# Optimization experiments

Measured on AMD Instinct MI355X. Metric: run time of the kernel, lower is better.

The kernel has to match this reference:

```python
import jax, jax.numpy as jnp
import numpy as np
import math

B, NV, L = 64, 21, 2048
PATCH, STRIDE = 16, 8
PNUM = (L - PATCH) // STRIDE + 1  # 255 patches
D, H, NDIM = 128, 256, 2
PRED = 96
EPS = 1e-5
SCALE = 1.0 / math.sqrt(NDIM)  # MultiHeadEMA scale = sqrt(1/ndim)
# patch gather indices: [PNUM, PATCH]
PIDX = np.arange(PNUM)[:, None] * STRIDE + np.arange(PATCH)[None, :]


def setup_inputs() -> dict:
    key = jax.random.key(0)
    ks = jax.random.split(key, 24)
    nrm = lambda k, shape, std: std * jax.random.normal(k, shape, jnp.float32)
    inp = {}
    inp['x'] = jax.random.normal(ks[0], (B, NV, L), jnp.float32)
    # LEMencoder feature_projection: LEMblock(PATCH -> H -> D)
    inp['fp_w1'] = nrm(ks[1], (PATCH, H), 0.1)
    inp['fp_b1'] = jnp.zeros((H,), jnp.float32)
    inp['fp_w2'] = nrm(ks[2], (H, D), 0.1)
    inp['fp_b2'] = jnp.zeros((D,), jnp.float32)
    inp['fp_wr'] = nrm(ks[3], (PATCH, D), 0.1)
    inp['fp_br'] = jnp.zeros((D,), jnp.float32)
    inp['fp_g'] = jnp.ones((D,), jnp.float32)
    inp['fp_be'] = jnp.zeros((D,), jnp.float32)
    # 2 stacked encoder LEMblocks (D -> D -> D), leading layer axis
    inp['enc_w1'] = nrm(ks[4], (2, D, D), 0.05)
    inp['enc_b1'] = jnp.zeros((2, D), jnp.float32)
    inp['enc_w2'] = nrm(ks[5], (2, D, D), 0.05)
    inp['enc_b2'] = jnp.zeros((2, D), jnp.float32)
    inp['enc_wr'] = nrm(ks[6], (2, D, D), 0.05)
    inp['enc_br'] = jnp.zeros((2, D), jnp.float32)
    inp['enc_g'] = jnp.ones((2, D), jnp.float32)
    inp['enc_be'] = jnp.zeros((2, D), jnp.float32)
    # MultiHeadEMA params (unidirectional: kernel_dim == D)
    inp['ema_delta'] = nrm(ks[7], (D, NDIM, 1), 0.2)
    inp['ema_alpha'] = nrm(ks[8], (D, NDIM, 1), 0.2)
    val = jnp.array([1.0, -1.0], jnp.float32).reshape(1, NDIM, 1)  # +1/-1 alternating init
    inp['ema_beta'] = nrm(ks[9], (D, NDIM, 1), 0.02) + val
    inp['ema_gamma'] = nrm(ks[10], (D, NDIM), 1.0)
    inp['ema_omega'] = nrm(ks[11], (D,), 1.0)
    # Flatten_Head (shared): Linear(D*PNUM -> PRED)
    inp['head_w'] = nrm(ks[12], (D * PNUM, PRED), 0.02)
    inp['head_b'] = jnp.zeros((PRED,), jnp.float32)
    return inp


def _lemblock(x, w1, b1, w2, b2, wr, br, g, be):
    h = jax.nn.relu(x @ w1 + b1) @ w2 + b2
    y = h + (x @ wr + br)
    mu = jnp.mean(y, axis=-1, keepdims=True)
    var = jnp.mean(jnp.square(y - mu), axis=-1, keepdims=True)
    return g * (y - mu) * jax.lax.rsqrt(var + EPS) + be


def reference(x, fp_w1, fp_b1, fp_w2, fp_b2, fp_wr, fp_br, fp_g, fp_be,
              enc_w1, enc_b1, enc_w2, enc_b2, enc_wr, enc_br, enc_g, enc_be,
              ema_delta, ema_alpha, ema_beta, ema_gamma, ema_omega,
              head_w, head_b):
    # patching: [B, NV, L] -> [B*NV, PNUM, PATCH]
    z = x[:, :, PIDX].reshape(B * NV, PNUM, PATCH)
    # LEMencoder
    z = _lemblock(z, fp_w1, fp_b1, fp_w2, fp_b2, fp_wr, fp_br, fp_g, fp_be)
    for i in range(enc_w1.shape[0]):
        z = _lemblock(z, enc_w1[i], enc_b1[i], enc_w2[i], enc_b2[i],
                      enc_wr[i], enc_br[i], enc_g[i], enc_be[i])
    # MultiHeadEMA over patch (time) axis; input [Time=PNUM, Batch=B*NV, Channel=D]
    t = jnp.transpose(z, (1, 0, 2))
    residual = t * ema_omega
    xc = jnp.transpose(t, (1, 2, 0))  # [BN, D, PNUM]
    p = jax.nn.sigmoid(ema_delta)           # [D, N, 1]
    q = 1.0 - p * jax.nn.sigmoid(ema_alpha)  # [D, N, 1]
    vander = jnp.arange(PNUM, dtype=jnp.float32)[None, None, :] * jnp.log(q)  # [D, N, PNUM]
    kern = p * ema_beta * jnp.exp(vander)
    k = jnp.einsum('dnl,dn->dl', kern, ema_gamma * SCALE)  # [D, PNUM]
    n2 = 2 * PNUM
    out = jnp.fft.irfft(jnp.fft.rfft(xc, n=n2) * jnp.fft.rfft(k, n=n2), n=n2)[..., :PNUM]
    out = jax.nn.silu(jnp.transpose(out, (2, 0, 1)) + residual)  # [PNUM, BN, D]
    # Flatten_Head (shared): [B, NV, D, PNUM] -> flatten(-2) -> linear
    u = jnp.transpose(out, (1, 2, 0)).reshape(B, NV, D * PNUM)
    return u @ head_w + head_b  # [B, NV, PRED]
```

## Files before the change

### kernel.cpp

```cpp
#include <hip/hip_runtime.h>

typedef unsigned short u16;
typedef short bf8v __attribute__((ext_vector_type(8)));
typedef float f4v __attribute__((ext_vector_type(4)));
typedef float f16v __attribute__((ext_vector_type(16)));

#define DEV static __device__ __forceinline__

constexpr int BB   = 64;
constexpr int NV   = 21;
constexpr int BN   = BB * NV;
constexpr int PNUM = 255;
constexpr int D    = 128;
constexpr int PRED = 96;
constexpr int ROWS = BN * PNUM;
constexpr int KH   = D * PNUM;
constexpr int CH   = 30;
constexpr int KPC  = KH / CH;
constexpr int HITER = KPC / 32;
constexpr float EMA_SCALE = 0.70710678118654752440f;

DEV float bf2f(u16 h) { return __uint_as_float(((unsigned)h) << 16); }
DEV u16 f2bf(float f) {
  unsigned u = __float_as_uint(f);
  return (u16)((u + 0x7fffu + ((u >> 16) & 1u)) >> 16);
}
DEV unsigned pkbf2(float a, float b) {
  unsigned ua = __float_as_uint(a) + 0x8000u;
  unsigned ub = __float_as_uint(b) + 0x8000u;
  return __builtin_amdgcn_perm(ub, ua, 0x07060302u);
}
DEV bf8v mk4(unsigned a, unsigned b, unsigned c, unsigned d) {
  int4 t = {(int)a, (int)b, (int)c, (int)d};
  bf8v r;
  __builtin_memcpy(&r, &t, 16);
  return r;
}
DEV bf8v ld8(const u16* p) {
  bf8v r;
  __builtin_memcpy(&r, p, 16);
  return r;
}
DEV f4v mfma16(bf8v a, bf8v b, f4v c) {
  return __builtin_amdgcn_mfma_f32_16x16x32_bf16(a, b, c, 0, 0, 0);
}
DEV f16v mfma32(bf8v a, bf8v b, f16v c) {
  return __builtin_amdgcn_mfma_f32_32x32x16_bf16(a, b, c, 0, 0, 0);
}
DEV f16v zero16() {
  f16v r;
#pragma unroll
  for (int i = 0; i < 16; i++) r[i] = 0.f;
  return r;
}

#define FRG(pk, ks)                                                            \
  mk4(pk[(ks) >> 1][2 * ((ks) & 1)][0], pk[(ks) >> 1][2 * ((ks) & 1)][1],      \
      pk[(ks) >> 1][2 * ((ks) & 1) + 1][0], pk[(ks) >> 1][2 * ((ks) & 1) + 1][1])

__global__ void swz_all(
    const float* __restrict__ fw1, const float* __restrict__ fw2,
    const float* __restrict__ fwr, const float* __restrict__ ew1,
    const float* __restrict__ ew2, const float* __restrict__ ewr,
    const float* __restrict__ hw, u16* __restrict__ wb, u16* __restrict__ wsh) {
  int b = blockIdx.x;
  if (b >= 560) {
    int i = (b - 560) * 256 + threadIdx.x;
    if (i >= KH * PRED) return;
    int kp = i / PRED, n = i - kp * PRED;
    int l = kp >> 7, d = kp & 127;
    wsh[((size_t)(kp >> 3) * PRED + n) * 8 + (kp & 7)] =
        f2bf(hw[(size_t)(d * PNUM + l) * PRED + n]);
    return;
  }
  const float* src; u16* dst; int K, N, Kp;
  if (b < 32)       { src = fw1; dst = wb;          K = 16;  N = 256; Kp = 32; }
  else if (b < 160) { b -= 32;  src = fw2; dst = wb + 8192;  K = 256; N = 128; Kp = 256; }
  else if (b < 176) { b -= 160; src = fwr; dst = wb + 40960; K = 16;  N = 128; Kp = 32; }
  else {
    int e = (b - 176) >> 6; b = (b - 176) & 63;
    int l = e / 3, w = e - 3 * l;
    const float* basep = (w == 0) ? ew1 : (w == 1) ? ew2 : ewr;
    src = basep + (size_t)l * 16384;
    dst = wb + 45056 + e * 16384;
    K = 128; N = 128; Kp = 128;
  }
  int i = b * 256 + threadIdx.x;
  if (i >= Kp * N) return;
  int k = i / N, n = i - k * N;
  int np = (n & ~12) | ((n & 4) << 1) | ((n & 8) >> 1);
  u16 v = (k < K) ? f2bf(src[(size_t)k * N + np]) : (u16)0;
  dst[((size_t)(k >> 3) * N + n) * 8 + (k & 7)] = v;
}

__global__ __launch_bounds__(128, 2) void k_lem(
    const float* __restrict__ x,
    const u16* __restrict__ ws1, const float* __restrict__ b1,
    const u16* __restrict__ ws2, const u16* __restrict__ wsr,
    const float* __restrict__ b2, const float* __restrict__ br,
    const float* __restrict__ g, const float* __restrict__ be,
    const u16* __restrict__ wse, const float* __restrict__ eb1,
    const float* __restrict__ eb2, const float* __restrict__ ebr,
    const float* __restrict__ eg, const float* __restrict__ ebe,
    u16* __restrict__ zout) {
  __shared__ __align__(16) u16 zst[64 * 132];
  const int t = threadIdx.x;
  const int lane = t & 63, w = t >> 6;
  const int hh = lane >> 5, r5 = lane & 31;
  const int tile = blockIdx.x;
  const int row = tile * 64 + w * 32 + r5;

  bf8v azv;
  {
    unsigned R = (unsigned)row;
    unsigned bn = R / 255u;
    unsigned p = R - bn * 255u;
    const float* px = x + (size_t)bn * 2048u + p * 8u + hh * 8;
    float4 v0 = *(const float4*)px;
    float4 v1 = *(const float4*)(px + 4);
    azv = mk4(pkbf2(v0.x, v0.y), pkbf2(v0.z, v0.w),
              pkbf2(v1.x, v1.y), pkbf2(v1.z, v1.w));
  }

  unsigned hpk[8][4][2];
  unsigned zpk[4][4][2];

#pragma unroll
  for (int half = 0; half < 2; half++) {
    f16v a[4];
#pragma unroll
    for (int gg = 0; gg < 4; gg++) {
      bf8v wf = ld8(ws1 + ((size_t)(hh * 256 + (half * 4 + gg) * 32 + r5)) * 8);
      a[gg] = mfma32(wf, azv, zero16());
    }
#pragma unroll
    for (int gg = 0; gg < 4; gg++)
#pragma unroll
      for (int wq = 0; wq < 4; wq++) {
        int c0 = (half * 4 + gg) * 32 + ((wq >> 1) << 4) + ((wq & 1) << 2) + (hh << 3);
        float4 bv = *(const float4*)(b1 + c0);
        float v0 = fmaxf(a[gg][wq * 4 + 0] + bv.x, 0.f);
        float v1 = fmaxf(a[gg][wq * 4 + 1] + bv.y, 0.f);
        float v2 = fmaxf(a[gg][wq * 4 + 2] + bv.z, 0.f);
        float v3 = fmaxf(a[gg][wq * 4 + 3] + bv.w, 0.f);
        hpk[half * 4 + gg][wq][0] = pkbf2(v0, v1);
        hpk[half * 4 + gg][wq][1] = pkbf2(v2, v3);
      }
  }

  f16v acc[4];
  {
    {
      bf8v wr4[4];
#pragma unroll
      for (int gg = 0; gg < 4; gg++)
        wr4[gg] = ld8(wsr + ((size_t)(hh * 128 + gg * 32 + r5)) * 8);
#pragma unroll
      for (int gg = 0; gg < 4; gg++) acc[gg] = mfma32(wr4[gg], azv, zero16());
    }
    bf8v wq[2][4];
#pragma unroll
    for (int gg = 0; gg < 4; gg++)
      wq[0][gg] = ld8(ws2 + ((size_t)(hh * 128 + gg * 32 + r5)) * 8);
#pragma unroll
    for (int u = 0; u < 16; u++) {
      int cur = u & 1;
      if (u + 1 < 16) {
#pragma unroll
        for (int gg = 0; gg < 4; gg++)
          wq[cur ^ 1][gg] =
              ld8(ws2 + ((size_t)((2 * (u + 1) + hh) * 128 + gg * 32 + r5)) * 8);
      }
      bf8v bfr = FRG(hpk, u);
#pragma unroll
      for (int gg = 0; gg < 4; gg++) acc[gg] = mfma32(wq[cur][gg], bfr, acc[gg]);
    }
    float s = 0.f, s2 = 0.f;
#pragma unroll
    for (int gg = 0; gg < 4; gg++)
#pragma unroll
      for (int wq4 = 0; wq4 < 4; wq4++) {
        int c0 = gg * 32 + ((wq4 >> 1) << 4) + ((wq4 & 1) << 2) + (hh << 3);
        float4 bv2 = *(const float4*)(b2 + c0);
        float4 bvr = *(const float4*)(br + c0);
        acc[gg][wq4 * 4 + 0] += bv2.x + bvr.x;
        acc[gg][wq4 * 4 + 1] += bv2.y + bvr.y;
        acc[gg][wq4 * 4 + 2] += bv2.z + bvr.z;
        acc[gg][wq4 * 4 + 3] += bv2.w + bvr.w;
#pragma unroll
        for (int sidx = 0; sidx < 4; sidx++) {
          float v = acc[gg][wq4 * 4 + sidx];
          s += v; s2 += v * v;
        }
      }
    s += __shfl_xor(s, 32, 64); s2 += __shfl_xor(s2, 32, 64);
    float mean = s * (1.f / 128.f);
    float rstd = rsqrtf(s2 * (1.f / 128.f) - mean * mean + 1e-5f);
#pragma unroll
    for (int gg = 0; gg < 4; gg++)
#pragma unroll
      for (int wq4 = 0; wq4 < 4; wq4++) {
        int c0 = gg * 32 + ((wq4 >> 1) << 4) + ((wq4 & 1) << 2) + (hh << 3);
        float4 gv = *(const float4*)(g + c0);
        float4 bv = *(const float4*)(be + c0);
        float v0 = (acc[gg][wq4 * 4 + 0] - mean) * rstd * gv.x + bv.x;
        float v1 = (acc[gg][wq4 * 4 + 1] - mean) * rstd * gv.y + bv.y;
        float v2 = (acc[gg][wq4 * 4 + 2] - mean) * rstd * gv.z + bv.z;
        float v3 = (acc[gg][wq4 * 4 + 3] - mean) * rstd * gv.w + bv.w;
        zpk[gg][wq4][0] = pkbf2(v0, v1);
        zpk[gg][wq4][1] = pkbf2(v2, v3);
      }
  }

#pragma unroll 1
  for (int L = 0; L < 2; L++) {
    const u16* w1p = wse + (size_t)(L * 3 + 0) * 16384;
    const u16* w2p = wse + (size_t)(L * 3 + 1) * 16384;
    const u16* wrp = wse + (size_t)(L * 3 + 2) * 16384;
    unsigned hp2[4][4][2];
    {
      f16v a2[4];
#pragma unroll
      for (int gg = 0; gg < 4; gg++) a2[gg] = zero16();
      bf8v wq[2][4];
#pragma unroll
      for (int gg = 0; gg < 4; gg++)
        wq[0][gg] = ld8(w1p + ((size_t)(hh * 128 + gg * 32 + r5)) * 8);
#pragma unroll
      for (int u = 0; u < 8; u++) {
        int cur = u & 1;
        if (u + 1 < 8) {
#pragma unroll
          for (int gg = 0; gg < 4; gg++)
            wq[cur ^ 1][gg] =
                ld8(w1p + ((size_t)((2 * (u + 1) + hh) * 128 + gg * 32 + r5)) * 8);
        }
        bf8v bfr = FRG(zpk, u);
#pragma unroll
        for (int gg = 0; gg < 4; gg++) a2[gg] = mfma32(wq[cur][gg], bfr, a2[gg]);
      }
#pragma unroll
      for (int gg = 0; gg < 4; gg++)
#pragma unroll
        for (int wq4 = 0; wq4 < 4; wq4++) {
          int c0 = gg * 32 + ((wq4 >> 1) << 4) + ((wq4 & 1) << 2) + (hh << 3);
          float4 bv = *(const float4*)(eb1 + L * 128 + c0);
          float v0 = fmaxf(a2[gg][wq4 * 4 + 0] + bv.x, 0.f);
          float v1 = fmaxf(a2[gg][wq4 * 4 + 1] + bv.y, 0.f);
          float v2 = fmaxf(a2[gg][wq4 * 4 + 2] + bv.z, 0.f);
          float v3 = fmaxf(a2[gg][wq4 * 4 + 3] + bv.w, 0.f);
          hp2[gg][wq4][0] = pkbf2(v0, v1);
          hp2[gg][wq4][1] = pkbf2(v2, v3);
        }
    }
#pragma unroll
    for (int gg = 0; gg < 4; gg++) acc[gg] = zero16();
    {
      bf8v wq[2][4];
#pragma unroll
      for (int gg = 0; gg < 4; gg++)
        wq[0][gg] = ld8(w2p + ((size_t)(hh * 128 + gg * 32 + r5)) * 8);
#pragma unroll
      for (int u = 0; u < 8; u++) {
        int cur = u & 1;
        if (u + 1 < 8) {
#pragma unroll
          for (int gg = 0; gg < 4; gg++)
            wq[cur ^ 1][gg] =
                ld8(w2p + ((size_t)((2 * (u + 1) + hh) * 128 + gg * 32 + r5)) * 8);
        }
        bf8v bfr = FRG(hp2, u);
#pragma unroll
        for (int gg = 0; gg < 4; gg++) acc[gg] = mfma32(wq[cur][gg], bfr, acc[gg]);
      }
    }
    {
      bf8v wq[2][4];
#pragma unroll
      for (int gg = 0; gg < 4; gg++)
        wq[0][gg] = ld8(wrp + ((size_t)(hh * 128 + gg * 32 + r5)) * 8);
#pragma unroll
      for (int u = 0; u < 8; u++) {
        int cur = u & 1;
        if (u + 1 < 8) {
#pragma unroll
          for (int gg = 0; gg < 4; gg++)
            wq[cur ^ 1][gg] =
                ld8(wrp + ((size_t)((2 * (u + 1) + hh) * 128 + gg * 32 + r5)) * 8);
        }
        bf8v bfr = FRG(zpk, u);
#pragma unroll
        for (int gg = 0; gg < 4; gg++) acc[gg] = mfma32(wq[cur][gg], bfr, acc[gg]);
      }
    }
    float s = 0.f, s2 = 0.f;
#pragma unroll
    for (int gg = 0; gg < 4; gg++)
#pragma unroll
      for (int wq4 = 0; wq4 < 4; wq4++) {
        int c0 = gg * 32 + ((wq4 >> 1) << 4) + ((wq4 & 1) << 2) + (hh << 3);
        float4 bv2 = *(const float4*)(eb2 + L * 128 + c0);
        float4 bvr = *(const float4*)(ebr + L * 128 + c0);
        acc[gg][wq4 * 4 + 0] += bv2.x + bvr.x;
        acc[gg][wq4 * 4 + 1] += bv2.y + bvr.y;
        acc[gg][wq4 * 4 + 2] += bv2.z + bvr.z;
        acc[gg][wq4 * 4 + 3] += bv2.w + bvr.w;
#pragma unroll
        for (int sidx = 0; sidx < 4; sidx++) {
          float v = acc[gg][wq4 * 4 + sidx];
          s += v; s2 += v * v;
        }
      }
    s += __shfl_xor(s, 32, 64); s2 += __shfl_xor(s2, 32, 64);
    float mean = s * (1.f / 128.f);
    float rstd = rsqrtf(s2 * (1.f / 128.f) - mean * mean + 1e-5f);
#pragma unroll
    for (int gg = 0; gg < 4; gg++)
#pragma unroll
      for (int wq4 = 0; wq4 < 4; wq4++) {
        int c0 = gg * 32 + ((wq4 >> 1) << 4) + ((wq4 & 1) << 2) + (hh << 3);
        float4 gv = *(const float4*)(eg + L * 128 + c0);
        float4 bv = *(const float4*)(ebe + L * 128 + c0);
        float v0 = (acc[gg][wq4 * 4 + 0] - mean) * rstd * gv.x + bv.x;
        float v1 = (acc[gg][wq4 * 4 + 1] - mean) * rstd * gv.y + bv.y;
        float v2 = (acc[gg][wq4 * 4 + 2] - mean) * rstd * gv.z + bv.z;
        float v3 = (acc[gg][wq4 * 4 + 3] - mean) * rstd * gv.w + bv.w;
        unsigned plo = pkbf2(v0, v1), phi = pkbf2(v2, v3);
        if (L == 0) {
          zpk[gg][wq4][0] = plo;
          zpk[gg][wq4][1] = phi;
        } else {
          uint2 pv = {plo, phi};
          *(uint2*)(zst + (w * 32 + r5) * 132 + c0) = pv;
        }
      }
  }

#pragma unroll
  for (int it = 0; it < 8; it++) {
    int lu = it * 64 + lane;
    int rr = lu >> 4, seg = lu & 15;
    int orow = w * 32 + rr;
    *(uint4*)(zout + ((size_t)tile * 64 + orow) * 128 + seg * 8) =
        *(const uint4*)(zst + orow * 132 + seg * 8);
  }
}

__global__ __launch_bounds__(128) void k_ema(
    u16* __restrict__ z,
    const float* __restrict__ pdel, const float* __restrict__ palp,
    const float* __restrict__ pbet, const float* __restrict__ pgam,
    const float* __restrict__ pome) {
  __shared__ __align__(16) u16 zc[64 * 128];
  const int t = threadIdx.x;
  const int bn = blockIdx.x;
  float p0 = 1.f / (1.f + __expf(-pdel[t * 2 + 0]));
  float p1 = 1.f / (1.f + __expf(-pdel[t * 2 + 1]));
  float q0 = 1.f - p0 / (1.f + __expf(-palp[t * 2 + 0]));
  float q1 = 1.f - p1 / (1.f + __expf(-palp[t * 2 + 1]));
  float w0 = p0 * pbet[t * 2 + 0] * pgam[t * 2 + 0] * EMA_SCALE;
  float w1 = p1 * pbet[t * 2 + 1] * pgam[t * 2 + 1] * EMA_SCALE;
  float om = pome[t];
  float s0 = 0.f, s1 = 0.f;
  u16* slab = z + (size_t)bn * KH;

  uint4 pre[8];
#pragma unroll
  for (int k = 0; k < 8; k++) pre[k] = *(const uint4*)(slab + t * 8 + k * 1024);

  for (int ch = 0; ch < 4; ch++) {
    int nrow = (ch < 3) ? 64 : 63;
    int nval = nrow * 128;
    __syncthreads();
#pragma unroll
    for (int k = 0; k < 8; k++) {
      int i = t * 8 + k * 1024;
      if (i < nval) *(uint4*)(zc + i) = pre[k];
    }
    if (ch < 3) {
      int nn = (ch < 2) ? 8192 : 8064;
#pragma unroll
      for (int k = 0; k < 8; k++) {
        int i = t * 8 + k * 1024;
        if (i < nn) pre[k] = *(const uint4*)(slab + (ch + 1) * 8192 + i);
      }
    }
    __syncthreads();
    for (int j0 = 0; j0 < nrow; j0 += 8) {
      float xs[8];
#pragma unroll
      for (int jj = 0; jj < 8; jj++)
        if (j0 + jj < nrow) xs[jj] = bf2f(zc[(j0 + jj) * 128 + t]);
#pragma unroll
      for (int jj = 0; jj < 8; jj++)
        if (j0 + jj < nrow) {
          float xv = xs[jj];
          s0 = q0 * s0 + xv;
          s1 = q1 * s1 + xv;
          float v = w0 * s0 + w1 * s1 + om * xv;
          xs[jj] = v / (1.f + __expf(-v));
        }
#pragma unroll
      for (int jj = 0; jj < 8; jj++)
        if (j0 + jj < nrow)
          zc[(j0 + jj) * 128 + t] = (u16)((__float_as_uint(xs[jj]) + 0x8000u) >> 16);
    }
    __syncthreads();
#pragma unroll
    for (int k = 0; k < 8; k++) {
      int i = t * 8 + k * 1024;
      if (i < nval) *(uint4*)(slab + ch * 8192 + i) = *(const uint4*)(zc + i);
    }
  }
}

__global__ __launch_bounds__(256) void k_head(
    const u16* __restrict__ u, const u16* __restrict__ whs, float* __restrict__ part) {
  const int t = threadIdx.x;
  const int lane = t & 63, wid = t >> 6;
  const int quad = lane >> 4, lc = lane & 15;
  const int tile = blockIdx.x;
  const int ch = blockIdx.y;
  const int m0 = tile * 64 + wid * 16;
  const u16* Ab = u + (size_t)(m0 + lc) * KH + (size_t)ch * KPC;
  const int g0 = ch * (KPC / 8);
  f4v acc[6];
#pragma unroll
  for (int n = 0; n < 6; n++) acc[n] = (f4v){0.f, 0.f, 0.f, 0.f};
  bf8v a_nxt = ld8(Ab + quad * 8);
  bf8v b_nxt[6];
#pragma unroll
  for (int n = 0; n < 6; n++)
    b_nxt[n] = ld8(whs + ((size_t)(g0 + quad) * PRED + n * 16 + lc) * 8);
  for (int ks = 0; ks < HITER; ks++) {
    bf8v a_cur = a_nxt;
    bf8v b_cur[6];
#pragma unroll
    for (int n = 0; n < 6; n++) b_cur[n] = b_nxt[n];
    if (ks < HITER - 1) {
      a_nxt = ld8(Ab + (ks + 1) * 32 + quad * 8);
#pragma unroll
      for (int n = 0; n < 6; n++)
        b_nxt[n] = ld8(whs + ((size_t)(g0 + (ks + 1) * 4 + quad) * PRED + n * 16 + lc) * 8);
    }
#pragma unroll
    for (int n = 0; n < 6; n++) acc[n] = mfma16(a_cur, b_cur[n], acc[n]);
  }
#pragma unroll
  for (int n = 0; n < 6; n++) {
    int col = n * 16 + lc;
#pragma unroll
    for (int r = 0; r < 4; r++)
      part[((size_t)ch * BN + m0 + quad * 4 + r) * PRED + col] = acc[n][r];
  }
}

__global__ __launch_bounds__(256) void k_red(
    const float* __restrict__ part, const float* __restrict__ hb, float* __restrict__ out) {
  int i = blockIdx.x * 256 + threadIdx.x;
  if (i >= BN * PRED) return;
  int row = i / PRED, col = i - row * PRED;
  float s = hb[col];
#pragma unroll 5
  for (int c = 0; c < CH; c++) s += part[((size_t)c * BN + row) * PRED + col];
  out[i] = s;
}

extern "C" void kernel_launch(void* const* d_in, const int* in_sizes, int n_in,
                              void* d_out, int out_size, void* d_ws, size_t ws_size,
                              hipStream_t stream) {
  const float* x      = (const float*)d_in[0];
  const float* fp_w1  = (const float*)d_in[1];
  const float* fp_b1  = (const float*)d_in[2];
  const float* fp_w2  = (const float*)d_in[3];
  const float* fp_b2  = (const float*)d_in[4];
  const float* fp_wr  = (const float*)d_in[5];
  const float* fp_br  = (const float*)d_in[6];
  const float* fp_g   = (const float*)d_in[7];
  const float* fp_be  = (const float*)d_in[8];
  const float* enc_w1 = (const float*)d_in[9];
  const float* enc_b1 = (const float*)d_in[10];
  const float* enc_w2 = (const float*)d_in[11];
  const float* enc_b2 = (const float*)d_in[12];
  const float* enc_wr = (const float*)d_in[13];
  const float* enc_br = (const float*)d_in[14];
  const float* enc_g  = (const float*)d_in[15];
  const float* enc_be = (const float*)d_in[16];
  const float* e_del  = (const float*)d_in[17];
  const float* e_alp  = (const float*)d_in[18];
  const float* e_bet  = (const float*)d_in[19];
  const float* e_gam  = (const float*)d_in[20];
  const float* e_om   = (const float*)d_in[21];
  const float* head_w = (const float*)d_in[22];
  const float* head_b = (const float*)d_in[23];

  char* base = (char*)d_ws;
  u16* z3 = (u16*)base;
  const size_t EZB = (size_t)ROWS * 128 * 2;
  float* part = (float*)(base + EZB);
  const size_t PARTB = (size_t)CH * BN * PRED * 4;
  u16* wb = (u16*)(base + EZB + PARTB);
  u16* ws1 = wb;
  u16* ws2 = wb + 8192;
  u16* wsr = wb + 40960;
  u16* wse = wb + 45056;
  u16* wsh = wb + 143360;

  swz_all<<<560 + (KH * PRED + 255) / 256, 256, 0, stream>>>(
      fp_w1, fp_w2, fp_wr, enc_w1, enc_w2, enc_wr, head_w, wb, wsh);

  k_lem<<<ROWS / 64, 128, 0, stream>>>(x, ws1, fp_b1, ws2, wsr, fp_b2, fp_br, fp_g, fp_be,
                                       wse, enc_b1, enc_b2, enc_br, enc_g, enc_be, z3);
  k_ema<<<BN, 128, 0, stream>>>(z3, e_del, e_alp, e_bet, e_gam, e_om);
  k_head<<<dim3(21, CH), 256, 0, stream>>>(z3, wsh, part);
  k_red<<<(BN * PRED + 255) / 256, 256, 0, stream>>>(part, head_b, (float*)d_out);
}
```

Before: 426.3 us.

## Pack MFMA B-fragments eagerly and drop EMA chunk prefetch registers

In the fused encoder kernel, activations are now packed straight into bf8v MFMA operand fragments right after each epilogue, so no separate per-step gather macro runs inside the matmul loops. This is meant to cut register shuffling and live ranges. In the EMA kernel, the register-based prefetch of the next 64-row chunk is removed in favour of a plain global-to-LDS copy per chunk with an extra barrier. That lowers register pressure but stops overlapping global loads with the sequential scan.

```diff
diff --git a/kernel.cpp b/kernel.cpp
--- a/kernel.cpp
+++ b/kernel.cpp
@@ -53,10 +53,6 @@
   for (int i = 0; i < 16; i++) r[i] = 0.f;
   return r;
 }
-
-#define FRG(pk, ks)                                                            \
-  mk4(pk[(ks) >> 1][2 * ((ks) & 1)][0], pk[(ks) >> 1][2 * ((ks) & 1)][1],      \
-      pk[(ks) >> 1][2 * ((ks) & 1) + 1][0], pk[(ks) >> 1][2 * ((ks) & 1) + 1][1])
 
 __global__ void swz_all(
     const float* __restrict__ fw1, const float* __restrict__ fw2,
@@ -122,8 +118,8 @@
               pkbf2(v1.x, v1.y), pkbf2(v1.z, v1.w));
   }
 
-  unsigned hpk[8][4][2];
-  unsigned zpk[4][4][2];
+  bf8v hfrag[16];
+  bf8v zfrag[8];
 
 #pragma unroll
   for (int half = 0; half < 2; half++) {
@@ -134,7 +130,8 @@
       a[gg] = mfma32(wf, azv, zero16());
     }
 #pragma unroll
-    for (int gg = 0; gg < 4; gg++)
+    for (int gg = 0; gg < 4; gg++) {
+      unsigned pk[4][2];
 #pragma unroll
       for (int wq = 0; wq < 4; wq++) {
         int c0 = (half * 4 + gg) * 32 + ((wq >> 1) << 4) + ((wq & 1) << 2) + (hh << 3);
@@ -143,9 +140,12 @@
         float v1 = fmaxf(a[gg][wq * 4 + 1] + bv.y, 0.f);
         float v2 = fmaxf(a[gg][wq * 4 + 2] + bv.z, 0.f);
         float v3 = fmaxf(a[gg][wq * 4 + 3] + bv.w, 0.f);
-        hpk[half * 4 + gg][wq][0] = pkbf2(v0, v1);
-        hpk[half * 4 + gg][wq][1] = pkbf2(v2, v3);
-      }
+        pk[wq][0] = pkbf2(v0, v1);
+        pk[wq][1] = pkbf2(v2, v3);
+      }
+      hfrag[(half * 4 + gg) * 2 + 0] = mk4(pk[0][0], pk[0][1], pk[1][0], pk[1][1]);
+      hfrag[(half * 4 + gg) * 2 + 1] = mk4(pk[2][0], pk[2][1], pk[3][0], pk[3][1]);
+    }
   }
 
   f16v acc[4];
@@ -171,9 +171,8 @@
           wq[cur ^ 1][gg] =
               ld8(ws2 + ((size_t)((2 * (u + 1) + hh) * 128 + gg * 32 + r5)) * 8);
       }
-      bf8v bfr = FRG(hpk, u);
-#pragma unroll
-      for (int gg = 0; gg < 4; gg++) acc[gg] = mfma32(wq[cur][gg], bfr, acc[gg]);
+#pragma unroll
+      for (int gg = 0; gg < 4; gg++) acc[gg] = mfma32(wq[cur][gg], hfrag[u], acc[gg]);
     }
     float s = 0.f, s2 = 0.f;
 #pragma unroll
@@ -197,7 +196,8 @@
     float mean = s * (1.f / 128.f);
     float rstd = rsqrtf(s2 * (1.f / 128.f) - mean * mean + 1e-5f);
 #pragma unroll
-    for (int gg = 0; gg < 4; gg++)
+    for (int gg = 0; gg < 4; gg++) {
+      unsigned pk[4][2];
 #pragma unroll
       for (int wq4 = 0; wq4 < 4; wq4++) {
         int c0 = gg * 32 + ((wq4 >> 1) << 4) + ((wq4 & 1) << 2) + (hh << 3);
@@ -207,9 +207,12 @@
         float v1 = (acc[gg][wq4 * 4 + 1] - mean) * rstd * gv.y + bv.y;
         float v2 = (acc[gg][wq4 * 4 + 2] - mean) * rstd * gv.z + bv.z;
         float v3 = (acc[gg][wq4 * 4 + 3] - mean) * rstd * gv.w + bv.w;
-        zpk[gg][wq4][0] = pkbf2(v0, v1);
-        zpk[gg][wq4][1] = pkbf2(v2, v3);
-      }
+        pk[wq4][0] = pkbf2(v0, v1);
+        pk[wq4][1] = pkbf2(v2, v3);
+      }
+      zfrag[gg * 2 + 0] = mk4(pk[0][0], pk[0][1], pk[1][0], pk[1][1]);
+      zfrag[gg * 2 + 1] = mk4(pk[2][0], pk[2][1], pk[3][0], pk[3][1]);
+    }
   }
 
 #pragma unroll 1
@@ -217,7 +220,7 @@
     const u16* w1p = wse + (size_t)(L * 3 + 0) * 16384;
     const u16* w2p = wse + (size_t)(L * 3 + 1) * 16384;
     const u16* wrp = wse + (size_t)(L * 3 + 2) * 16384;
-    unsigned hp2[4][4][2];
+    bf8v hfr2[8];
     {
       f16v a2[4];
 #pragma unroll
@@ -235,12 +238,12 @@
             wq[cur ^ 1][gg] =
                 ld8(w1p + ((size_t)((2 * (u + 1) + hh) * 128 + gg * 32 + r5)) * 8);
         }
-        bf8v bfr = FRG(zpk, u);
-#pragma unroll
-        for (int gg = 0; gg < 4; gg++) a2[gg] = mfma32(wq[cur][gg], bfr, a2[gg]);
-      }
-#pragma unroll
-      for (int gg = 0; gg < 4; gg++)
+#pragma unroll
+        for (int gg = 0; gg < 4; gg++) a2[gg] = mfma32(wq[cur][gg], zfrag[u], a2[gg]);
+      }
+#pragma unroll
+      for (int gg = 0; gg < 4; gg++) {
+        unsigned pk[4][2];
 #pragma unroll
         for (int wq4 = 0; wq4 < 4; wq4++) {
           int c0 = gg * 32 + ((wq4 >> 1) << 4) + ((wq4 & 1) << 2) + (hh << 3);
@@ -249,9 +252,12 @@
           float v1 = fmaxf(a2[gg][wq4 * 4 + 1] + bv.y, 0.f);
           float v2 = fmaxf(a2[gg][wq4 * 4 + 2] + bv.z, 0.f);
           float v3 = fmaxf(a2[gg][wq4 * 4 + 3] + bv.w, 0.f);
-          hp2[gg][wq4][0] = pkbf2(v0, v1);
-          hp2[gg][wq4][1] = pkbf2(v2, v3);
-        }
+          pk[wq4][0] = pkbf2(v0, v1);
+          pk[wq4][1] = pkbf2(v2, v3);
+        }
+        hfr2[gg * 2 + 0] = mk4(pk[0][0], pk[0][1], pk[1][0], pk[1][1]);
+        hfr2[gg * 2 + 1] = mk4(pk[2][0], pk[2][1], pk[3][0], pk[3][1]);
+      }
     }
 #pragma unroll
     for (int gg = 0; gg < 4; gg++) acc[gg] = zero16();
@@ -269,9 +275,8 @@
             wq[cur ^ 1][gg] =
                 ld8(w2p + ((size_t)((2 * (u + 1) + hh) * 128 + gg * 32 + r5)) * 8);
         }
-        bf8v bfr = FRG(hp2, u);
-#pragma unroll
-        for (int gg = 0; gg < 4; gg++) acc[gg] = mfma32(wq[cur][gg], bfr, acc[gg]);
+#pragma unroll
+        for (int gg = 0; gg < 4; gg++) acc[gg] = mfma32(wq[cur][gg], hfr2[u], acc[gg]);
       }
     }
     {
@@ -288,9 +293,8 @@
             wq[cur ^ 1][gg] =
                 ld8(wrp + ((size_t)((2 * (u + 1) + hh) * 128 + gg * 32 + r5)) * 8);
         }
-        bf8v bfr = FRG(zpk, u);
-#pragma unroll
-        for (int gg = 0; gg < 4; gg++) acc[gg] = mfma32(wq[cur][gg], bfr, acc[gg]);
+#pragma unroll
+        for (int gg = 0; gg < 4; gg++) acc[gg] = mfma32(wq[cur][gg], zfrag[u], acc[gg]);
       }
     }
     float s = 0.f, s2 = 0.f;
@@ -315,7 +319,8 @@
     float mean = s * (1.f / 128.f);
     float rstd = rsqrtf(s2 * (1.f / 128.f) - mean * mean + 1e-5f);
 #pragma unroll
-    for (int gg = 0; gg < 4; gg++)
+    for (int gg = 0; gg < 4; gg++) {
+      unsigned pk[4][2];
 #pragma unroll
       for (int wq4 = 0; wq4 < 4; wq4++) {
         int c0 = gg * 32 + ((wq4 >> 1) << 4) + ((wq4 & 1) << 2) + (hh << 3);
@@ -326,14 +331,19 @@
         float v2 = (acc[gg][wq4 * 4 + 2] - mean) * rstd * gv.z + bv.z;
         float v3 = (acc[gg][wq4 * 4 + 3] - mean) * rstd * gv.w + bv.w;
         unsigned plo = pkbf2(v0, v1), phi = pkbf2(v2, v3);
-        if (L == 0) {
-          zpk[gg][wq4][0] = plo;
-          zpk[gg][wq4][1] = phi;
-        } else {
+        if (L == 1) {
           uint2 pv = {plo, phi};
           *(uint2*)(zst + (w * 32 + r5) * 132 + c0) = pv;
-        }
-      }
+        } else {
+          pk[wq4][0] = plo;
+          pk[wq4][1] = phi;
+        }
+      }
+      if (L == 0) {
+        zfrag[gg * 2 + 0] = mk4(pk[0][0], pk[0][1], pk[1][0], pk[1][1]);
+        zfrag[gg * 2 + 1] = mk4(pk[2][0], pk[2][1], pk[3][0], pk[3][1]);
+      }
+    }
   }
 
 #pragma unroll
@@ -364,27 +374,11 @@
   float s0 = 0.f, s1 = 0.f;
   u16* slab = z + (size_t)bn * KH;
 
-  uint4 pre[8];
-#pragma unroll
-  for (int k = 0; k < 8; k++) pre[k] = *(const uint4*)(slab + t * 8 + k * 1024);
-
   for (int ch = 0; ch < 4; ch++) {
     int nrow = (ch < 3) ? 64 : 63;
     int nval = nrow * 128;
-    __syncthreads();
-#pragma unroll
-    for (int k = 0; k < 8; k++) {
-      int i = t * 8 + k * 1024;
-      if (i < nval) *(uint4*)(zc + i) = pre[k];
-    }
-    if (ch < 3) {
-      int nn = (ch < 2) ? 8192 : 8064;
-#pragma unroll
-      for (int k = 0; k < 8; k++) {
-        int i = t * 8 + k * 1024;
-        if (i < nn) pre[k] = *(const uint4*)(slab + (ch + 1) * 8192 + i);
-      }
-    }
+    for (int i = t * 8; i < nval; i += 128 * 8)
+      *(uint4*)(zc + i) = *(const uint4*)(slab + ch * 8192 + i);
     __syncthreads();
     for (int j0 = 0; j0 < nrow; j0 += 8) {
       float xs[8];
@@ -406,11 +400,9 @@
           zc[(j0 + jj) * 128 + t] = (u16)((__float_as_uint(xs[jj]) + 0x8000u) >> 16);
     }
     __syncthreads();
-#pragma unroll
-    for (int k = 0; k < 8; k++) {
-      int i = t * 8 + k * 1024;
-      if (i < nval) *(uint4*)(slab + ch * 8192 + i) = *(const uint4*)(zc + i);
-    }
+    for (int i = t * 8; i < nval; i += 128 * 8)
+      *(uint4*)(slab + ch * 8192 + i) = *(const uint4*)(zc + i);
+    __syncthreads();
   }
 }
 
```

Measured after the change: 433.6 us. About the same (+1.7%).
